# Kernel optimization log

Hardware: AMD Instinct MI355X
Metric: run time of the kernel (lower is better)

The kernel has to match this reference:

```python
import jax, jax.numpy as jnp
import numpy as np

H = 128          # hidden_size
EF = 2           # expansion_factor
E = H * EF       # expanded hidden size
K = 4            # conv kernel size
R = 8            # dt_rank = ceil(128/16)
L = 2            # num_layers
BATCH = 2
SEQ = 1024
EPS = 1e-5


def rmsnorm(x, w):
    return x * jax.lax.rsqrt(jnp.mean(x * x, axis=-1, keepdims=True) + EPS) * w


def causal_conv1d(x, w, b):
    # x: (b, l, E); w: (E, 1, K) depthwise; left-pad K-1 => causal, output len l
    xt = jnp.transpose(x, (0, 2, 1))  # (b, E, l)
    out = jax.lax.conv_general_dilated(
        xt, w, window_strides=(1,), padding=[(K - 1, 0)],
        dimension_numbers=("NCH", "OIH", "NCH"), feature_group_count=E)
    out = out + b[None, :, None]
    return jnp.transpose(out, (0, 2, 1))


def sscan(xc, delta, A, Bm, Cm, Dp):
    # xc, delta: (b,l,E); A: (E,n); Bm, Cm: (b,l,n); Dp: (E,)
    deltaA = jnp.exp(jnp.einsum('bld,dn->bldn', delta, A))          # (b,l,E,n)
    deltaBx = jnp.einsum('bld,bln,bld->bldn', delta, Bm, xc)        # (b,l,E,n)

    def step(h, inp):
        dA_t, dBx_t, C_t = inp           # (b,E,n), (b,E,n), (b,n)
        h = dA_t * h + dBx_t
        y = jnp.einsum('bdn,bn->bd', h, C_t)
        return h, y

    b = xc.shape[0]
    h0 = jnp.zeros((b, E, A.shape[1]), dtype=xc.dtype)
    _, ys = jax.lax.scan(
        step, h0,
        (jnp.transpose(deltaA, (1, 0, 2, 3)),
         jnp.transpose(deltaBx, (1, 0, 2, 3)),
         jnp.transpose(Cm, (1, 0, 2))))
    y = jnp.transpose(ys, (1, 0, 2))     # (b,l,E)
    return y + Dp * xc


def mamba_block(x, in_w, in_b, out_w, out_b, pl_w, pl_b, dt_w, dt_b,
                conv_w, conv_b, A_log, Dp):
    xz = x @ in_w + in_b                 # (b,l,2E)
    xc, skip = jnp.split(xz, [E], axis=-1)
    xc = jax.nn.silu(causal_conv1d(xc, conv_w, conv_b))
    # ssm
    A = -jnp.exp(A_log)                  # (E,H)
    dbc = xc @ pl_w + pl_b               # (b,l,R+2H)
    delta, Bm, Cm = jnp.split(dbc, [R, R + H], axis=-1)
    delta = jax.nn.softplus(delta @ dt_w + dt_b)   # (b,l,E)
    y = sscan(xc, delta, A, Bm, Cm, Dp)
    y = y * jax.nn.silu(skip)
    return y @ out_w + out_b


def forward(x, in_w, in_b, out_w, out_b, pl_w, pl_b, dt_w, dt_b,
            conv_w, conv_b, A_log, Dp, norm_w, final_norm_w):
    for i in range(L):
        x = mamba_block(rmsnorm(x, norm_w[i]), in_w[i], in_b[i], out_w[i],
                        out_b[i], pl_w[i], pl_b[i], dt_w[i], dt_b[i],
                        conv_w[i], conv_b[i], A_log[i], Dp[i]) + x
    return rmsnorm(x, final_norm_w)


def setup_inputs() -> dict:
    key = jax.random.key(0)
    ks = jax.random.split(key, 12)
    s = 0.02
    x = jax.random.normal(ks[0], (BATCH, SEQ, H), dtype=jnp.float32)
    in_w = jax.random.normal(ks[1], (L, H, 2 * E)) * s
    in_b = jnp.zeros((L, 2 * E))
    out_w = jax.random.normal(ks[2], (L, E, H)) * s
    out_b = jnp.zeros((L, H))
    pl_w = jax.random.normal(ks[3], (L, E, R + 2 * H)) * s
    pl_b = jnp.zeros((L, R + 2 * H))
    dt_w = jax.random.normal(ks[4], (L, R, E)) * s
    dt_b = jnp.zeros((L, E))
    conv_w = jax.random.normal(ks[5], (L, E, 1, K)) * (1.0 / np.sqrt(K))
    conv_b = jnp.zeros((L, E))
    A_log = jnp.broadcast_to(jnp.log(jnp.arange(1, H + 1, dtype=jnp.float32)),
                             (L, E, H))
    Dp = jnp.ones((L, E))
    norm_w = jnp.ones((L, H))
    final_norm_w = jnp.ones((H,))
    return {"x": x, "in_w": in_w, "in_b": in_b, "out_w": out_w,
            "out_b": out_b, "pl_w": pl_w, "pl_b": pl_b, "dt_w": dt_w,
            "dt_b": dt_b, "conv_w": conv_w, "conv_b": conv_b,
            "A_log": A_log, "Dp": Dp, "norm_w": norm_w,
            "final_norm_w": final_norm_w}


def reference(x, in_w, in_b, out_w, out_b, pl_w, pl_b, dt_w, dt_b,
              conv_w, conv_b, A_log, Dp, norm_w, final_norm_w):
    return forward(x, in_w, in_b, out_w, out_b, pl_w, pl_b, dt_w, dt_b,
                   conv_w, conv_b, A_log, Dp, norm_w, final_norm_w)
```

## Files before the change

kernel.cpp:

```cpp
#include <hip/hip_runtime.h>
#include <hip/hip_bf16.h>

#define HH 128
#define EE 256
#define KK 4
#define RR 8
#define LL 2
#define BB 2
#define SS 1024
#define BT (BB*SS)
#define NJ (RR+2*HH)
#define GG 16
#define CH (SS/GG)
#define EPS 1e-5f
#define LOG2E 1.44269504088896f

__device__ __forceinline__ float silu_f(float v) {
    return v / (1.0f + __expf(-v));
}

__global__ __launch_bounds__(256) void k_prep(
    const float* __restrict__ plw, const float* __restrict__ plb,
    const float* __restrict__ dtw, const float* __restrict__ dtb,
    const float* __restrict__ Alog,
    float* __restrict__ Wdt, float* __restrict__ bdt,
    float* __restrict__ Antab)
{
    const int blk = blockIdx.x;
    if (blk < 8) {
        const int l = blk >> 2, q = blk & 3;
        const int j = threadIdx.x;
        const float* dtwl = dtw + (size_t)l * RR * EE;
        const float* plwl = plw + (size_t)l * EE * NJ;
        float wr[RR];
        #pragma unroll
        for (int r = 0; r < RR; r++) wr[r] = dtwl[r * EE + j];
        float* Wl = Wdt + (size_t)l * EE * EE;
        for (int e = q * 64; e < q * 64 + 64; e++) {
            float a = 0.0f;
            #pragma unroll
            for (int r = 0; r < RR; r++) a += plwl[(size_t)e * NJ + r] * wr[r];
            Wl[(size_t)e * EE + j] = a;
        }
        if (q == 0) {
            float a = dtb[l * EE + j];
            #pragma unroll
            for (int r = 0; r < RR; r++) a += plb[l * NJ + r] * wr[r];
            bdt[l * EE + j] = a;
        }
    } else {
        const int blk2 = blk - 8;
        const int l = blk2 >> 2, q = blk2 & 3;
        const size_t base = (size_t)l * EE * HH;
        for (int i = 0; i < 32; i++) {
            const int flat = q * 8192 + i * 256 + threadIdx.x;
            Antab[base + flat] = -__expf(Alog[base + flat]) * LOG2E;
        }
    }
}

__global__ __launch_bounds__(512) void k_norm_inproj(
    const float* __restrict__ xin, const float* __restrict__ inw,
    const float* __restrict__ inb, const float* __restrict__ nw,
    float* __restrict__ xz)
{
    __shared__ float xn[8][128];
    const int bt0 = blockIdx.x * 8;
    const int tid = threadIdx.x;
    {
        const int t = tid >> 6, lane = tid & 63;
        const float2 xv = *(const float2*)(xin + (size_t)(bt0 + t) * HH + lane * 2);
        float ss = xv.x*xv.x + xv.y*xv.y;
        #pragma unroll
        for (int m = 32; m >= 1; m >>= 1) ss += __shfl_xor(ss, m);
        const float rs = rsqrtf(ss * (1.0f / HH) + EPS);
        const float2 wv = *(const float2*)(nw + lane * 2);
        xn[t][lane*2+0] = xv.x * rs * wv.x;
        xn[t][lane*2+1] = xv.y * rs * wv.y;
    }
    __syncthreads();
    const int j = tid;
    float acc[8];
    const float bj = inb[j];
    #pragma unroll
    for (int t = 0; t < 8; t++) acc[t] = bj;
    float w0n = inw[0*512 + j], w1n = inw[1*512 + j];
    float w2n = inw[2*512 + j], w3n = inw[3*512 + j];
    for (int k4 = 0; k4 < 32; k4++) {
        const float w0 = w0n, w1 = w1n, w2 = w2n, w3 = w3n;
        if (k4 < 31) {
            const int k = (k4 + 1) * 4;
            w0n = inw[(k+0)*512 + j]; w1n = inw[(k+1)*512 + j];
            w2n = inw[(k+2)*512 + j]; w3n = inw[(k+3)*512 + j];
        }
        const int k = k4 * 4;
        #pragma unroll
        for (int t = 0; t < 8; t++) {
            const float4 xv = *(const float4*)(&xn[t][k]);
            acc[t] += w0*xv.x + w1*xv.y + w2*xv.z + w3*xv.w;
        }
    }
    #pragma unroll
    for (int t = 0; t < 8; t++) xz[(size_t)(bt0 + t) * 512 + j] = acc[t];
}

__global__ __launch_bounds__(512) void k_cbd(
    const float* __restrict__ xz, const float* __restrict__ cw,
    const float* __restrict__ cb, const float* __restrict__ plw,
    const float* __restrict__ plb, const float* __restrict__ Wdt,
    const float* __restrict__ bdt,
    float* __restrict__ xcT, float* __restrict__ BC4,
    float* __restrict__ deltaT, float* __restrict__ sT)
{
    __shared__ float xcb[8][256];
    const int bt0 = blockIdx.x * 8;
    const int tid = threadIdx.x;
    {
        const int e = tid & 255, hf = tid >> 8;
        const int ts = bt0 + hf * 4;
        const float w0 = cw[e*4+0], w1 = cw[e*4+1], w2 = cw[e*4+2], w3 = cw[e*4+3];
        const float bias = cb[e];
        const float* xp = xz + (size_t)ts * 512 + e;
        const bool first = ((ts & (SS-1)) == 0);
        float xm3 = first ? 0.0f : xp[-3*512];
        float xm2 = first ? 0.0f : xp[-2*512];
        float xm1 = first ? 0.0f : xp[-1*512];
        float xcv[4];
        #pragma unroll
        for (int i = 0; i < 4; i++) {
            const float x0 = xp[i*512];
            const float v = bias + w3*x0 + w2*xm1 + w1*xm2 + w0*xm3;
            const float o = silu_f(v);
            xcv[i] = o;
            xcb[hf*4 + i][e] = o;
            xm3 = xm2; xm2 = xm1; xm1 = x0;
        }
        *(float4*)(xcT + (size_t)e * BT + ts) =
            make_float4(xcv[0], xcv[1], xcv[2], xcv[3]);
    }
    __syncthreads();
    const int j = tid & 255, path = tid >> 8;
    if (path == 0) {
        const int nn = j & 127, isC = j >> 7;
        const float* wp = plw + RR + isC * HH + nn;
        float acc[8];
        const float bj = plb[RR + isC * HH + nn];
        #pragma unroll
        for (int t = 0; t < 8; t++) acc[t] = bj;
        float w0n = wp[0*NJ], w1n = wp[1*NJ], w2n = wp[2*NJ], w3n = wp[3*NJ];
        for (int e4 = 0; e4 < 64; e4++) {
            const float w0 = w0n, w1 = w1n, w2 = w2n, w3 = w3n;
            if (e4 < 63) {
                const int e = (e4 + 1) * 4;
                w0n = wp[(size_t)(e+0)*NJ]; w1n = wp[(size_t)(e+1)*NJ];
                w2n = wp[(size_t)(e+2)*NJ]; w3n = wp[(size_t)(e+3)*NJ];
            }
            const int e = e4 * 4;
            #pragma unroll
            for (int t = 0; t < 8; t++) {
                const float4 xv = *(const float4*)(&xcb[t][e]);
                acc[t] += w0*xv.x + w1*xv.y + w2*xv.z + w3*xv.w;
            }
        }
        const int tq0 = bt0 >> 2;
        float* p0 = BC4 + ((size_t)tq0 * 128 + nn) * 8 + isC * 4;
        *(float4*)p0 = make_float4(acc[0], acc[1], acc[2], acc[3]);
        float* p1 = BC4 + ((size_t)(tq0 + 1) * 128 + nn) * 8 + isC * 4;
        *(float4*)p1 = make_float4(acc[4], acc[5], acc[6], acc[7]);
    } else {
        const float* wp = Wdt + j;
        float acc[8];
        const float bj = bdt[j];
        #pragma unroll
        for (int t = 0; t < 8; t++) acc[t] = bj;
        float w0n = wp[0*EE], w1n = wp[1*EE], w2n = wp[2*EE], w3n = wp[3*EE];
        for (int e4 = 0; e4 < 64; e4++) {
            const float w0 = w0n, w1 = w1n, w2 = w2n, w3 = w3n;
            if (e4 < 63) {
                const int e = (e4 + 1) * 4;
                w0n = wp[(size_t)(e+0)*EE]; w1n = wp[(size_t)(e+1)*EE];
                w2n = wp[(size_t)(e+2)*EE]; w3n = wp[(size_t)(e+3)*EE];
            }
            const int e = e4 * 4;
            #pragma unroll
            for (int t = 0; t < 8; t++) {
                const float4 xv = *(const float4*)(&xcb[t][e]);
                acc[t] += w0*xv.x + w1*xv.y + w2*xv.z + w3*xv.w;
            }
        }
        float spv[8], sv[8];
        #pragma unroll
        for (int t = 0; t < 8; t++) {
            const float d = acc[t];
            const float sp = (d > 15.0f) ? d : log1pf(__expf(d));
            spv[t] = sp;
            sv[t] = sp * xcb[t][j];
        }
        float* drp = deltaT + (size_t)j * BT + bt0;
        *(float4*)(drp)     = make_float4(spv[0], spv[1], spv[2], spv[3]);
        *(float4*)(drp + 4) = make_float4(spv[4], spv[5], spv[6], spv[7]);
        float* srp = sT + (size_t)j * BT + bt0;
        *(float4*)(srp)     = make_float4(sv[0], sv[1], sv[2], sv[3]);
        *(float4*)(srp + 4) = make_float4(sv[4], sv[5], sv[6], sv[7]);
    }
}

__global__ __launch_bounds__(128, 4) void k_scanA(
    const float* __restrict__ BC4, const float* __restrict__ deltaT,
    const float* __restrict__ sT, const float* __restrict__ Antab,
    float* __restrict__ hchain, float* __restrict__ dsum)
{
    const int blk = blockIdx.x;
    const int wgid = (blk & 7) * 256 + (blk >> 3);
    const int eq = wgid & 63;
    const int r0 = wgid >> 6;
    const int b = r0 >> 4;
    const int g = r0 & 15;
    const int e0 = eq * 4;
    const int n = threadIdx.x;
    const int t0 = g * CH;

    float An[4], h[4], cum[4];
    #pragma unroll
    for (int ee = 0; ee < 4; ee++) {
        An[ee] = Antab[(e0 + ee) * HH + n];
        h[ee] = 0.0f; cum[ee] = 0.0f;
    }
    const float* bc = BC4 + ((size_t)((b * 256 + g * 16) * 128 + n)) * 8;
    const float* dr[4]; const float* sr[4];
    #pragma unroll
    for (int ee = 0; ee < 4; ee++) {
        dr[ee] = deltaT + (size_t)(e0 + ee) * BT + b * SS + t0;
        sr[ee] = sT + (size_t)(e0 + ee) * BT + b * SS + t0;
    }
    float4 pB = *(const float4*)(bc);
    float4 pd[4], ps[4];
    #pragma unroll
    for (int ee = 0; ee < 4; ee++) {
        pd[ee] = *(const float4*)dr[ee];
        ps[ee] = *(const float4*)sr[ee];
    }
    for (int qq = 0; qq < 16; qq++) {
        const float4 cB = pB;
        float4 cd[4], cs[4];
        #pragma unroll
        for (int ee = 0; ee < 4; ee++) { cd[ee] = pd[ee]; cs[ee] = ps[ee]; }
        if (qq < 15) {
            const size_t off = (size_t)(qq + 1) * 1024;
            pB = *(const float4*)(bc + off);
            const int t = (qq + 1) * 4;
            #pragma unroll
            for (int ee = 0; ee < 4; ee++) {
                pd[ee] = *(const float4*)(dr[ee] + t);
                ps[ee] = *(const float4*)(sr[ee] + t);
            }
        }
        #pragma unroll
        for (int ee = 0; ee < 4; ee++) {
            float a;
            a = exp2f(cd[ee].x*An[ee]); h[ee] = a*h[ee] + cs[ee].x*cB.x;
            a = exp2f(cd[ee].y*An[ee]); h[ee] = a*h[ee] + cs[ee].y*cB.y;
            a = exp2f(cd[ee].z*An[ee]); h[ee] = a*h[ee] + cs[ee].z*cB.z;
            a = exp2f(cd[ee].w*An[ee]); h[ee] = a*h[ee] + cs[ee].w*cB.w;
            cum[ee] += (cd[ee].x + cd[ee].y) + (cd[ee].z + cd[ee].w);
        }
    }
    #pragma unroll
    for (int ee = 0; ee < 4; ee++)
        hchain[(size_t)(((b * EE + e0 + ee) * GG) + g) * 128 + n] = h[ee];
    if (n == 0) {
        #pragma unroll
        for (int ee = 0; ee < 4; ee++)
            dsum[(b * EE + e0 + ee) * GG + g] = cum[ee];
    }
}

__global__ __launch_bounds__(128) void k_combine(
    const float* __restrict__ Antab, const float* __restrict__ dsum,
    float* __restrict__ hchain)
{
    const int be = blockIdx.x;
    const int e = be & 255;
    const int n = threadIdx.x;
    const float An = Antab[e * HH + n];
    const size_t base = (size_t)be * GG * 128 + n;
    float he[GG], ds[GG];
    #pragma unroll
    for (int g = 0; g < GG; g++) he[g] = hchain[base + (size_t)g * 128];
    #pragma unroll
    for (int g = 0; g < GG; g++) ds[g] = dsum[be * GG + g];
    float h = 0.0f;
    #pragma unroll
    for (int g = 0; g < GG; g++) {
        hchain[base + (size_t)g * 128] = h;
        h = exp2f(An * ds[g]) * h + he[g];
    }
}

__global__ __launch_bounds__(128, 4) void k_scanB(
    const float* __restrict__ BC4, const float* __restrict__ deltaT,
    const float* __restrict__ sT, const float* __restrict__ Antab,
    const float* __restrict__ hchain, float* __restrict__ yT)
{
    __shared__ float part[4][16][68];
    __shared__ float ybuf[4][CH];
    const int blk = blockIdx.x;
    const int wgid = (blk & 7) * 256 + (blk >> 3);
    const int eq = wgid & 63;
    const int r0 = wgid >> 6;
    const int b = r0 >> 4;
    const int g = r0 & 15;
    const int e0 = eq * 4;
    const int n = threadIdx.x;
    const int t0 = g * CH;

    float An[4], h[4];
    #pragma unroll
    for (int ee = 0; ee < 4; ee++) {
        An[ee] = Antab[(e0 + ee) * HH + n];
        h[ee] = hchain[(size_t)(((b * EE + e0 + ee) * GG) + g) * 128 + n];
    }
    const float* bc = BC4 + ((size_t)((b * 256 + g * 16) * 128 + n)) * 8;
    const float* dr[4]; const float* sr[4];
    #pragma unroll
    for (int ee = 0; ee < 4; ee++) {
        dr[ee] = deltaT + (size_t)(e0 + ee) * BT + b * SS + t0;
        sr[ee] = sT + (size_t)(e0 + ee) * BT + b * SS + t0;
    }
    float4 pB = *(const float4*)(bc);
    float4 pC = *(const float4*)(bc + 4);
    float4 pd[4], ps[4];
    #pragma unroll
    for (int ee = 0; ee < 4; ee++) {
        pd[ee] = *(const float4*)dr[ee];
        ps[ee] = *(const float4*)sr[ee];
    }
    const int tl = n >> 3, jj = n & 7;
    for (int sc = 0; sc < 4; sc++) {
        #pragma unroll
        for (int q = 0; q < 4; q++) {
            const int qq = sc * 4 + q;
            const float4 cB = pB, cC = pC;
            float4 cd[4], cs[4];
            #pragma unroll
            for (int ee = 0; ee < 4; ee++) { cd[ee] = pd[ee]; cs[ee] = ps[ee]; }
            if (qq < 15) {
                const size_t off = (size_t)(qq + 1) * 1024;
                pB = *(const float4*)(bc + off);
                pC = *(const float4*)(bc + off + 4);
                const int t = (qq + 1) * 4;
                #pragma unroll
                for (int ee = 0; ee < 4; ee++) {
                    pd[ee] = *(const float4*)(dr[ee] + t);
                    ps[ee] = *(const float4*)(sr[ee] + t);
                }
            }
            #pragma unroll
            for (int ee = 0; ee < 4; ee++) {
                float a;
                a = exp2f(cd[ee].x*An[ee]); h[ee] = a*h[ee] + cs[ee].x*cB.x;
                part[ee][q*4+0][n] = h[ee]*cC.x;
                a = exp2f(cd[ee].y*An[ee]); h[ee] = a*h[ee] + cs[ee].y*cB.y;
                part[ee][q*4+1][n] = h[ee]*cC.y;
                a = exp2f(cd[ee].z*An[ee]); h[ee] = a*h[ee] + cs[ee].z*cB.z;
                part[ee][q*4+2][n] = h[ee]*cC.z;
                a = exp2f(cd[ee].w*An[ee]); h[ee] = a*h[ee] + cs[ee].w*cB.w;
                part[ee][q*4+3][n] = h[ee]*cC.w;
            }
        }
        __syncthreads();
        #pragma unroll
        for (int ee = 0; ee < 4; ee++) {
            float s0 = 0, s1 = 0, s2 = 0, s3 = 0;
            #pragma unroll
            for (int i = 0; i < 4; i++) {
                const float4 p = *(const float4*)(&part[ee][tl][jj*16 + i*4]);
                s0 += p.x; s1 += p.y; s2 += p.z; s3 += p.w;
            }
            float r = (s0 + s1) + (s2 + s3);
            r += __shfl_xor(r, 1); r += __shfl_xor(r, 2); r += __shfl_xor(r, 4);
            if (jj == 0) ybuf[ee][sc*16 + tl] = r;
        }
        __syncthreads();
    }
    {
        const int ee = n >> 5, tt = n & 31;
        float* yp = yT + (size_t)(e0 + ee) * BT + b * SS + t0;
        yp[tt] = ybuf[ee][tt];
        yp[tt + 32] = ybuf[ee][tt + 32];
    }
}

__global__ __launch_bounds__(256) void k_gate(
    const float* __restrict__ yT, const float* __restrict__ xcT,
    const float* __restrict__ xz, const float* __restrict__ Dp,
    const float* __restrict__ ow, const float* __restrict__ ob,
    const float* __restrict__ resin, float* __restrict__ xres)
{
    __shared__ float gs[8][256];
    __shared__ float p2[8][128];
    const int bt0 = blockIdx.x * 8;
    const int tid = threadIdx.x;
    {
        const int e = tid;
        const float dp = Dp[e];
        const float* yp = yT + (size_t)e * BT + bt0;
        const float* xp = xcT + (size_t)e * BT + bt0;
        #pragma unroll
        for (int tq = 0; tq < 2; tq++) {
            const float4 y4 = *(const float4*)(yp + tq * 4);
            const float4 x4 = *(const float4*)(xp + tq * 4);
            float sk;
            sk = xz[(size_t)(bt0 + tq*4 + 0) * 512 + 256 + e];
            gs[tq*4+0][e] = (y4.x + dp * x4.x) * silu_f(sk);
            sk = xz[(size_t)(bt0 + tq*4 + 1) * 512 + 256 + e];
            gs[tq*4+1][e] = (y4.y + dp * x4.y) * silu_f(sk);
            sk = xz[(size_t)(bt0 + tq*4 + 2) * 512 + 256 + e];
            gs[tq*4+2][e] = (y4.z + dp * x4.z) * silu_f(sk);
            sk = xz[(size_t)(bt0 + tq*4 + 3) * 512 + 256 + e];
            gs[tq*4+3][e] = (y4.w + dp * x4.w) * silu_f(sk);
        }
    }
    __syncthreads();
    const int j = tid & 127;
    const int kh = tid >> 7;
    float acc[8];
    #pragma unroll
    for (int t = 0; t < 8; t++) acc[t] = 0.0f;
    const int eb = kh * 128;
    float w0n = ow[(eb+0)*HH + j], w1n = ow[(eb+1)*HH + j];
    float w2n = ow[(eb+2)*HH + j], w3n = ow[(eb+3)*HH + j];
    for (int e4 = 0; e4 < 32; e4++) {
        const float w0 = w0n, w1 = w1n, w2 = w2n, w3 = w3n;
        if (e4 < 31) {
            const int e = eb + (e4 + 1) * 4;
            w0n = ow[(e+0)*HH + j]; w1n = ow[(e+1)*HH + j];
            w2n = ow[(e+2)*HH + j]; w3n = ow[(e+3)*HH + j];
        }
        const int e = eb + e4 * 4;
        #pragma unroll
        for (int t = 0; t < 8; t++) {
            const float4 g4 = *(const float4*)(&gs[t][e]);
            acc[t] += w0*g4.x + w1*g4.y + w2*g4.z + w3*g4.w;
        }
    }
    if (kh == 1) {
        #pragma unroll
        for (int t = 0; t < 8; t++) p2[t][j] = acc[t];
    }
    __syncthreads();
    if (kh == 0) {
        const float bj = ob[j];
        #pragma unroll
        for (int t = 0; t < 8; t++) {
            const float r = acc[t] + p2[t][j] + bj
                          + resin[(size_t)(bt0 + t) * HH + j];
            xres[(size_t)(bt0 + t) * HH + j] = r;
        }
    }
}

__global__ __launch_bounds__(256) void k_gate_final(
    const float* __restrict__ yT, const float* __restrict__ xcT,
    const float* __restrict__ xz, const float* __restrict__ Dp,
    const float* __restrict__ ow, const float* __restrict__ ob,
    const float* __restrict__ resin, const float* __restrict__ fw,
    float* __restrict__ out)
{
    __shared__ float gs[8][256];
    __shared__ float p2[8][132];
    const int bt0 = blockIdx.x * 8;
    const int tid = threadIdx.x;
    {
        const int e = tid;
        const float dp = Dp[e];
        const float* yp = yT + (size_t)e * BT + bt0;
        const float* xp = xcT + (size_t)e * BT + bt0;
        #pragma unroll
        for (int tq = 0; tq < 2; tq++) {
            const float4 y4 = *(const float4*)(yp + tq * 4);
            const float4 x4 = *(const float4*)(xp + tq * 4);
            float sk;
            sk = xz[(size_t)(bt0 + tq*4 + 0) * 512 + 256 + e];
            gs[tq*4+0][e] = (y4.x + dp * x4.x) * silu_f(sk);
            sk = xz[(size_t)(bt0 + tq*4 + 1) * 512 + 256 + e];
            gs[tq*4+1][e] = (y4.y + dp * x4.y) * silu_f(sk);
            sk = xz[(size_t)(bt0 + tq*4 + 2) * 512 + 256 + e];
            gs[tq*4+2][e] = (y4.z + dp * x4.z) * silu_f(sk);
            sk = xz[(size_t)(bt0 + tq*4 + 3) * 512 + 256 + e];
            gs[tq*4+3][e] = (y4.w + dp * x4.w) * silu_f(sk);
        }
    }
    __syncthreads();
    const int j = tid & 127;
    const int kh = tid >> 7;
    {
        float acc[8];
        #pragma unroll
        for (int t = 0; t < 8; t++) acc[t] = 0.0f;
        const int eb = kh * 128;
        float w0n = ow[(eb+0)*HH + j], w1n = ow[(eb+1)*HH + j];
        float w2n = ow[(eb+2)*HH + j], w3n = ow[(eb+3)*HH + j];
        for (int e4 = 0; e4 < 32; e4++) {
            const float w0 = w0n, w1 = w1n, w2 = w2n, w3 = w3n;
            if (e4 < 31) {
                const int e = eb + (e4 + 1) * 4;
                w0n = ow[(e+0)*HH + j]; w1n = ow[(e+1)*HH + j];
                w2n = ow[(e+2)*HH + j]; w3n = ow[(e+3)*HH + j];
            }
            const int e = eb + e4 * 4;
            #pragma unroll
            for (int t = 0; t < 8; t++) {
                const float4 g4 = *(const float4*)(&gs[t][e]);
                acc[t] += w0*g4.x + w1*g4.y + w2*g4.z + w3*g4.w;
            }
        }
        if (kh == 1) {
            #pragma unroll
            for (int t = 0; t < 8; t++) p2[t][j] = acc[t];
        }
        __syncthreads();
        if (kh == 0) {
            const float bj = ob[j];
            #pragma unroll
            for (int t = 0; t < 8; t++) {
                const float r = acc[t] + p2[t][j] + bj
                              + resin[(size_t)(bt0 + t) * HH + j];
                p2[t][j] = r;
            }
        }
    }
    __syncthreads();
    {
        const int t = tid >> 5, lane = tid & 31;
        const float4 v = *(const float4*)(&p2[t][lane * 4]);
        float ss = v.x*v.x + v.y*v.y + v.z*v.z + v.w*v.w;
        ss += __shfl_xor(ss, 16); ss += __shfl_xor(ss, 8);
        ss += __shfl_xor(ss, 4);  ss += __shfl_xor(ss, 2);
        ss += __shfl_xor(ss, 1);
        const float rs = rsqrtf(ss * (1.0f / HH) + EPS);
        const float4 w = *(const float4*)(fw + lane * 4);
        float4 o;
        o.x = v.x * rs * w.x; o.y = v.y * rs * w.y;
        o.z = v.z * rs * w.z; o.w = v.w * rs * w.w;
        *(float4*)(out + (size_t)(bt0 + t) * HH + lane * 4) = o;
    }
}

extern "C" void kernel_launch(void* const* d_in, const int* in_sizes, int n_in,
                              void* d_out, int out_size, void* d_ws, size_t ws_size,
                              hipStream_t stream)
{
    const float* x      = (const float*)d_in[0];
    const float* in_w   = (const float*)d_in[1];
    const float* in_b   = (const float*)d_in[2];
    const float* out_w  = (const float*)d_in[3];
    const float* out_b  = (const float*)d_in[4];
    const float* pl_w   = (const float*)d_in[5];
    const float* pl_b   = (const float*)d_in[6];
    const float* dt_w   = (const float*)d_in[7];
    const float* dt_b   = (const float*)d_in[8];
    const float* conv_w = (const float*)d_in[9];
    const float* conv_b = (const float*)d_in[10];
    const float* A_log  = (const float*)d_in[11];
    const float* Dp     = (const float*)d_in[12];
    const float* norm_w = (const float*)d_in[13];
    const float* fnw    = (const float*)d_in[14];

    float* ws     = (float*)d_ws;
    float* xres   = ws;
    float* xz     = xres   + 262144;
    float* xcT    = xz     + 1048576;
    float* BC4    = xcT    + 524288;
    float* deltaT = BC4    + 524288;
    float* sT     = deltaT + 524288;
    float* yT     = sT     + 524288;
    float* hchain = yT     + 524288;
    float* dsum   = hchain + 1048576;
    float* Wdt    = dsum   + 8192;
    float* bdt    = Wdt    + 131072;
    float* Antab  = bdt    + 512;

    k_prep<<<16, 256, 0, stream>>>(pl_w, pl_b, dt_w, dt_b, A_log,
                                   Wdt, bdt, Antab);

    for (int l = 0; l < LL; l++) {
        const float* resin = (l == 0) ? x : xres;
        k_norm_inproj<<<BT/8, 512, 0, stream>>>(
            resin, in_w + (size_t)l*HH*2*EE, in_b + (size_t)l*2*EE,
            norm_w + (size_t)l*HH, xz);
        k_cbd<<<BT/8, 512, 0, stream>>>(
            xz, conv_w + (size_t)l*EE*KK, conv_b + (size_t)l*EE,
            pl_w + (size_t)l*EE*NJ, pl_b + (size_t)l*NJ,
            Wdt + (size_t)l*EE*EE, bdt + (size_t)l*EE,
            xcT, BC4, deltaT, sT);
        k_scanA<<<BB*GG*(EE/4), 128, 0, stream>>>(
            BC4, deltaT, sT, Antab + (size_t)l*EE*HH, hchain, dsum);
        k_combine<<<BB*EE, 128, 0, stream>>>(
            Antab + (size_t)l*EE*HH, dsum, hchain);
        k_scanB<<<BB*GG*(EE/4), 128, 0, stream>>>(
            BC4, deltaT, sT, Antab + (size_t)l*EE*HH, hchain, yT);
        if (l < LL - 1) {
            k_gate<<<BT/8, 256, 0, stream>>>(
                yT, xcT, xz, Dp + (size_t)l*EE,
                out_w + (size_t)l*EE*HH, out_b + (size_t)l*HH, resin, xres);
        } else {
            k_gate_final<<<BT/8, 256, 0, stream>>>(
                yT, xcT, xz, Dp + (size_t)l*EE,
                out_w + (size_t)l*EE*HH, out_b + (size_t)l*HH, xres,
                fnw, (float*)d_out);
        }
    }
}
```

Baseline: 244.9 us.

## Restructure chunked scan into local scan plus carry-in correction pass

Replaces the three-pass chunked scan (local state pass, serial combine, full rescan) with two passes. The first computes each chunk's outputs from a zero initial state and also records the chunk's end state and delta sum. The second adds, for chunks after the first, the carried-in state's contribution to y, using an exponential of the running delta sum times the prefix-combined incoming state. This drops the separate combine kernel and the second full recurrence, but every fix block must recompute the prefix over earlier chunks. The delta/s prefetch also becomes two-deep.

```diff
diff --git a/kernel.cpp b/kernel.cpp
--- a/kernel.cpp
+++ b/kernel.cpp
@@ -205,102 +205,11 @@
     }
 }
 
-__global__ __launch_bounds__(128, 4) void k_scanA(
+__global__ __launch_bounds__(128, 4) void k_scan_local(
     const float* __restrict__ BC4, const float* __restrict__ deltaT,
     const float* __restrict__ sT, const float* __restrict__ Antab,
-    float* __restrict__ hchain, float* __restrict__ dsum)
-{
-    const int blk = blockIdx.x;
-    const int wgid = (blk & 7) * 256 + (blk >> 3);
-    const int eq = wgid & 63;
-    const int r0 = wgid >> 6;
-    const int b = r0 >> 4;
-    const int g = r0 & 15;
-    const int e0 = eq * 4;
-    const int n = threadIdx.x;
-    const int t0 = g * CH;
-
-    float An[4], h[4], cum[4];
-    #pragma unroll
-    for (int ee = 0; ee < 4; ee++) {
-        An[ee] = Antab[(e0 + ee) * HH + n];
-        h[ee] = 0.0f; cum[ee] = 0.0f;
-    }
-    const float* bc = BC4 + ((size_t)((b * 256 + g * 16) * 128 + n)) * 8;
-    const float* dr[4]; const float* sr[4];
-    #pragma unroll
-    for (int ee = 0; ee < 4; ee++) {
-        dr[ee] = deltaT + (size_t)(e0 + ee) * BT + b * SS + t0;
-        sr[ee] = sT + (size_t)(e0 + ee) * BT + b * SS + t0;
-    }
-    float4 pB = *(const float4*)(bc);
-    float4 pd[4], ps[4];
-    #pragma unroll
-    for (int ee = 0; ee < 4; ee++) {
-        pd[ee] = *(const float4*)dr[ee];
-        ps[ee] = *(const float4*)sr[ee];
-    }
-    for (int qq = 0; qq < 16; qq++) {
-        const float4 cB = pB;
-        float4 cd[4], cs[4];
-        #pragma unroll
-        for (int ee = 0; ee < 4; ee++) { cd[ee] = pd[ee]; cs[ee] = ps[ee]; }
-        if (qq < 15) {
-            const size_t off = (size_t)(qq + 1) * 1024;
-            pB = *(const float4*)(bc + off);
-            const int t = (qq + 1) * 4;
-            #pragma unroll
-            for (int ee = 0; ee < 4; ee++) {
-                pd[ee] = *(const float4*)(dr[ee] + t);
-                ps[ee] = *(const float4*)(sr[ee] + t);
-            }
-        }
-        #pragma unroll
-        for (int ee = 0; ee < 4; ee++) {
-            float a;
-            a = exp2f(cd[ee].x*An[ee]); h[ee] = a*h[ee] + cs[ee].x*cB.x;
-            a = exp2f(cd[ee].y*An[ee]); h[ee] = a*h[ee] + cs[ee].y*cB.y;
-            a = exp2f(cd[ee].z*An[ee]); h[ee] = a*h[ee] + cs[ee].z*cB.z;
-            a = exp2f(cd[ee].w*An[ee]); h[ee] = a*h[ee] + cs[ee].w*cB.w;
-            cum[ee] += (cd[ee].x + cd[ee].y) + (cd[ee].z + cd[ee].w);
-        }
-    }
-    #pragma unroll
-    for (int ee = 0; ee < 4; ee++)
-        hchain[(size_t)(((b * EE + e0 + ee) * GG) + g) * 128 + n] = h[ee];
-    if (n == 0) {
-        #pragma unroll
-        for (int ee = 0; ee < 4; ee++)
-            dsum[(b * EE + e0 + ee) * GG + g] = cum[ee];
-    }
-}
-
-__global__ __launch_bounds__(128) void k_combine(
-    const float* __restrict__ Antab, const float* __restrict__ dsum,
-    float* __restrict__ hchain)
-{
-    const int be = blockIdx.x;
-    const int e = be & 255;
-    const int n = threadIdx.x;
-    const float An = Antab[e * HH + n];
-    const size_t base = (size_t)be * GG * 128 + n;
-    float he[GG], ds[GG];
-    #pragma unroll
-    for (int g = 0; g < GG; g++) he[g] = hchain[base + (size_t)g * 128];
-    #pragma unroll
-    for (int g = 0; g < GG; g++) ds[g] = dsum[be * GG + g];
-    float h = 0.0f;
-    #pragma unroll
-    for (int g = 0; g < GG; g++) {
-        hchain[base + (size_t)g * 128] = h;
-        h = exp2f(An * ds[g]) * h + he[g];
-    }
-}
-
-__global__ __launch_bounds__(128, 4) void k_scanB(
-    const float* __restrict__ BC4, const float* __restrict__ deltaT,
-    const float* __restrict__ sT, const float* __restrict__ Antab,
-    const float* __restrict__ hchain, float* __restrict__ yT)
+    float* __restrict__ yT, float* __restrict__ hchain,
+    float* __restrict__ dsum)
 {
     __shared__ float part[4][16][68];
     __shared__ float ybuf[4][CH];
@@ -314,11 +223,11 @@
     const int n = threadIdx.x;
     const int t0 = g * CH;
 
-    float An[4], h[4];
+    float An[4], h[4], cum[4];
     #pragma unroll
     for (int ee = 0; ee < 4; ee++) {
         An[ee] = Antab[(e0 + ee) * HH + n];
-        h[ee] = hchain[(size_t)(((b * EE + e0 + ee) * GG) + g) * 128 + n];
+        h[ee] = 0.0f; cum[ee] = 0.0f;
     }
     const float* bc = BC4 + ((size_t)((b * 256 + g * 16) * 128 + n)) * 8;
     const float* dr[4]; const float* sr[4];
@@ -329,30 +238,35 @@
     }
     float4 pB = *(const float4*)(bc);
     float4 pC = *(const float4*)(bc + 4);
-    float4 pd[4], ps[4];
+    float4 pd[4][2], ps[4][2];
     #pragma unroll
     for (int ee = 0; ee < 4; ee++) {
-        pd[ee] = *(const float4*)dr[ee];
-        ps[ee] = *(const float4*)sr[ee];
+        pd[ee][0] = *(const float4*)dr[ee];
+        ps[ee][0] = *(const float4*)sr[ee];
+        pd[ee][1] = *(const float4*)(dr[ee] + 4);
+        ps[ee][1] = *(const float4*)(sr[ee] + 4);
     }
     const int tl = n >> 3, jj = n & 7;
     for (int sc = 0; sc < 4; sc++) {
         #pragma unroll
         for (int q = 0; q < 4; q++) {
             const int qq = sc * 4 + q;
+            const int slot = q & 1;
             const float4 cB = pB, cC = pC;
             float4 cd[4], cs[4];
             #pragma unroll
-            for (int ee = 0; ee < 4; ee++) { cd[ee] = pd[ee]; cs[ee] = ps[ee]; }
+            for (int ee = 0; ee < 4; ee++) { cd[ee] = pd[ee][slot]; cs[ee] = ps[ee][slot]; }
             if (qq < 15) {
                 const size_t off = (size_t)(qq + 1) * 1024;
                 pB = *(const float4*)(bc + off);
                 pC = *(const float4*)(bc + off + 4);
-                const int t = (qq + 1) * 4;
+            }
+            if (qq < 14) {
+                const int t = (qq + 2) * 4;
                 #pragma unroll
                 for (int ee = 0; ee < 4; ee++) {
-                    pd[ee] = *(const float4*)(dr[ee] + t);
-                    ps[ee] = *(const float4*)(sr[ee] + t);
+                    pd[ee][slot] = *(const float4*)(dr[ee] + t);
+                    ps[ee][slot] = *(const float4*)(sr[ee] + t);
                 }
             }
             #pragma unroll
@@ -366,6 +280,7 @@
                 part[ee][q*4+2][n] = h[ee]*cC.z;
                 a = exp2f(cd[ee].w*An[ee]); h[ee] = a*h[ee] + cs[ee].w*cB.w;
                 part[ee][q*4+3][n] = h[ee]*cC.w;
+                cum[ee] += (cd[ee].x + cd[ee].y) + (cd[ee].z + cd[ee].w);
             }
         }
         __syncthreads();
@@ -388,6 +303,111 @@
         float* yp = yT + (size_t)(e0 + ee) * BT + b * SS + t0;
         yp[tt] = ybuf[ee][tt];
         yp[tt + 32] = ybuf[ee][tt + 32];
+    }
+    #pragma unroll
+    for (int ee = 0; ee < 4; ee++)
+        hchain[(size_t)(((b * EE + e0 + ee) * GG) + g) * 128 + n] = h[ee];
+    if (n == 0) {
+        #pragma unroll
+        for (int ee = 0; ee < 4; ee++)
+            dsum[(b * EE + e0 + ee) * GG + g] = cum[ee];
+    }
+}
+
+__global__ __launch_bounds__(128, 4) void k_scan_fix(
+    const float* __restrict__ BC4, const float* __restrict__ deltaT,
+    const float* __restrict__ Antab, const float* __restrict__ hchain,
+    const float* __restrict__ dsum, float* __restrict__ yT)
+{
+    __shared__ float part[4][16][68];
+    __shared__ float ybuf[4][CH];
+    const int blk = blockIdx.x;
+    const int wgid = (blk & 7) * 240 + (blk >> 3);
+    const int eq = wgid & 63;
+    const int r0 = wgid >> 6;
+    const int b = r0 / 15;
+    const int g = 1 + (r0 % 15);
+    const int e0 = eq * 4;
+    const int n = threadIdx.x;
+    const int t0 = g * CH;
+
+    float An[4], wst[4], D[4];
+    #pragma unroll
+    for (int ee = 0; ee < 4; ee++) {
+        An[ee] = Antab[(e0 + ee) * HH + n];
+        wst[ee] = 0.0f; D[ee] = 0.0f;
+    }
+    {
+        for (int gp = 0; gp < g; gp++) {
+            #pragma unroll
+            for (int ee = 0; ee < 4; ee++) {
+                const float he = hchain[(size_t)(((b * EE + e0 + ee) * GG) + gp) * 128 + n];
+                const float ds = dsum[(b * EE + e0 + ee) * GG + gp];
+                wst[ee] = exp2f(An[ee] * ds) * wst[ee] + he;
+            }
+        }
+    }
+    const float* bc = BC4 + ((size_t)((b * 256 + g * 16) * 128 + n)) * 8;
+    const float* dr[4];
+    #pragma unroll
+    for (int ee = 0; ee < 4; ee++)
+        dr[ee] = deltaT + (size_t)(e0 + ee) * BT + b * SS + t0;
+
+    float4 pC = *(const float4*)(bc + 4);
+    float4 pd[4][2];
+    #pragma unroll
+    for (int ee = 0; ee < 4; ee++) {
+        pd[ee][0] = *(const float4*)dr[ee];
+        pd[ee][1] = *(const float4*)(dr[ee] + 4);
+    }
+    const int tl = n >> 3, jj = n & 7;
+    for (int sc = 0; sc < 4; sc++) {
+        #pragma unroll
+        for (int q = 0; q < 4; q++) {
+            const int qq = sc * 4 + q;
+            const int slot = q & 1;
+            const float4 cC = pC;
+            float4 cd[4];
+            #pragma unroll
+            for (int ee = 0; ee < 4; ee++) cd[ee] = pd[ee][slot];
+            if (qq < 15) {
+                const size_t off = (size_t)(qq + 1) * 1024;
+                pC = *(const float4*)(bc + off + 4);
+            }
+            if (qq < 14) {
+                const int t = (qq + 2) * 4;
+                #pragma unroll
+                for (int ee = 0; ee < 4; ee++)
+                    pd[ee][slot] = *(const float4*)(dr[ee] + t);
+            }
+            #pragma unroll
+            for (int ee = 0; ee < 4; ee++) {
+                D[ee] += cd[ee].x; part[ee][q*4+0][n] = exp2f(An[ee]*D[ee]) * wst[ee] * cC.x;
+                D[ee] += cd[ee].y; part[ee][q*4+1][n] = exp2f(An[ee]*D[ee]) * wst[ee] * cC.y;
+                D[ee] += cd[ee].z; part[ee][q*4+2][n] = exp2f(An[ee]*D[ee]) * wst[ee] * cC.z;
+                D[ee] += cd[ee].w; part[ee][q*4+3][n] = exp2f(An[ee]*D[ee]) * wst[ee] * cC.w;
+            }
+        }
+        __syncthreads();
+        #pragma unroll
+        for (int ee = 0; ee < 4; ee++) {
+            float s0 = 0, s1 = 0, s2 = 0, s3 = 0;
+            #pragma unroll
+            for (int i = 0; i < 4; i++) {
+                const float4 p = *(const float4*)(&part[ee][tl][jj*16 + i*4]);
+                s0 += p.x; s1 += p.y; s2 += p.z; s3 += p.w;
+            }
+            float r = (s0 + s1) + (s2 + s3);
+            r += __shfl_xor(r, 1); r += __shfl_xor(r, 2); r += __shfl_xor(r, 4);
+            if (jj == 0) ybuf[ee][sc*16 + tl] = r;
+        }
+        __syncthreads();
+    }
+    {
+        const int ee = n >> 5, tt = n & 31;
+        float* yp = yT + (size_t)(e0 + ee) * BT + b * SS + t0;
+        yp[tt] += ybuf[ee][tt];
+        yp[tt + 32] += ybuf[ee][tt + 32];
     }
 }
 
@@ -594,12 +614,10 @@
             pl_w + (size_t)l*EE*NJ, pl_b + (size_t)l*NJ,
             Wdt + (size_t)l*EE*EE, bdt + (size_t)l*EE,
             xcT, BC4, deltaT, sT);
-        k_scanA<<<BB*GG*(EE/4), 128, 0, stream>>>(
-            BC4, deltaT, sT, Antab + (size_t)l*EE*HH, hchain, dsum);
-        k_combine<<<BB*EE, 128, 0, stream>>>(
-            Antab + (size_t)l*EE*HH, dsum, hchain);
-        k_scanB<<<BB*GG*(EE/4), 128, 0, stream>>>(
-            BC4, deltaT, sT, Antab + (size_t)l*EE*HH, hchain, yT);
+        k_scan_local<<<BB*GG*(EE/4), 128, 0, stream>>>(
+            BC4, deltaT, sT, Antab + (size_t)l*EE*HH, yT, hchain, dsum);
+        k_scan_fix<<<BB*(GG-1)*(EE/4), 128, 0, stream>>>(
+            BC4, deltaT, Antab + (size_t)l*EE*HH, hchain, dsum, yT);
         if (l < LL - 1) {
             k_gate<<<BT/8, 256, 0, stream>>>(
                 yT, xcT, xz, Dp + (size_t)l*EE,
```

After: 255.1 us. 1.04x slower.
